# Kernel tuning notes

Measured on AMD Instinct MI355X. Metric: run time of the kernel, lower is better.

## Reference

```python
import jax, jax.numpy as jnp
import numpy as np
from jax import lax


def _conv1x1(x, w, b=None):
    # x: [N,C,H,W], w: [O,C]
    y = jnp.einsum('nchw,oc->nohw', x, w)
    if b is not None:
        y = y + b[None, :, None, None]
    return y


def _bn(x, g, b, rm, rv):
    # eval-mode BatchNorm2d, eps=1e-5 (torch default)
    inv = g / jnp.sqrt(rv + 1e-5)
    return x * inv[None, :, None, None] + (b - rm * inv)[None, :, None, None]


def setup_inputs() -> dict:
    key = jax.random.key(0)
    ks = jax.random.split(key, 32)
    N, C1, C2, H, W = 16, 256, 256, 64, 64
    mid = C2 // 16  # local_att reduction=16
    f32 = jnp.float32
    def nrm(k, shp, s=0.05):
        return s * jax.random.normal(k, shp, f32)
    return dict(
        x1=jax.random.normal(ks[0], (N, C1, H, W), f32),
        x2=jax.random.normal(ks[1], (N, C2, H, W), f32),
        conv1_w=nrm(ks[2], (C2, C1)), conv1_b=nrm(ks[3], (C2,)),
        conv2_w=nrm(ks[4], (C2, C2)), conv2_b=nrm(ks[5], (C2,)),
        conv3_w=nrm(ks[6], (C2, C2)), conv3_b=nrm(ks[7], (C2,)),
        conv4_w=nrm(ks[8], (C2, C2)), conv4_b=nrm(ks[9], (C2,)),
        conv4g_w=nrm(ks[10], (1, C2)), conv4g_b=nrm(ks[11], (1,)),
        bn_g=1.0 + nrm(ks[12], (C2,)), bn_b=nrm(ks[13], (C2,)),
        bn_rm=nrm(ks[14], (C2,)), bn_rv=1.0 + 0.1 * jax.random.uniform(ks[15], (C2,), f32),
        gamma=jax.random.normal(ks[16], (C2, 1, 1), f32), beta=jnp.zeros((C2, 1, 1), f32),
        gate_w=nrm(ks[17], (C2, C2)), gate_b=nrm(ks[18], (C2,)),
        dw_w=nrm(ks[19], (C2, 1, 3, 3)), dw_b=nrm(ks[20], (C2,)),
        interact_w=nrm(ks[21], (C2 // 4, C2 // 4)), interact_b=0.5 + nrm(ks[22], (C2 // 4,)),
        ca_w=nrm(ks[23], (1, 1, 5)),  # channel_att conv1d kernel, k=5 for C=256
        la1_w=nrm(ks[24], (mid, C2)),
        la_bn_g=1.0 + nrm(ks[25], (mid,)), la_bn_b=nrm(ks[26], (mid,)),
        la_bn_rm=nrm(ks[27], (mid,)), la_bn_rv=1.0 + 0.1 * jax.random.uniform(ks[28], (mid,), f32),
        fh_w=nrm(ks[29], (C2, mid)), fw_w=nrm(ks[30], (C2, mid)),
    )


def reference(x1, x2, conv1_w, conv1_b, conv2_w, conv2_b, conv3_w, conv3_b,
              conv4_w, conv4_b, conv4g_w, conv4g_b, bn_g, bn_b, bn_rm, bn_rv,
              gamma, beta, gate_w, gate_b, dw_w, dw_b, interact_w, interact_b,
              ca_w, la1_w, la_bn_g, la_bn_b, la_bn_rm, la_bn_rv, fh_w, fw_w):
    N, _, H, W = x1.shape
    C = conv1_w.shape[0]
    g1 = _conv1x1(x1, conv1_w, conv1_b)
    w1 = jax.nn.sigmoid(_bn(g1, bn_g, bn_b, bn_rm, bn_rv))
    g2 = _conv1x1(x2, conv2_w, conv2_b)
    w2 = jax.nn.sigmoid(_bn(g2, bn_g, bn_b, bn_rm, bn_rv))
    XG = g1 + g2

    # channel_att: GAP -> conv1d(k=5) across channels -> sigmoid gate
    y = XG.mean((2, 3))[:, None, :]  # [N,1,C]
    y = lax.conv_general_dilated(y, ca_w, (1,), [(2, 2)],
                                 dimension_numbers=('NCH', 'OIH', 'NCH'))
    temp = XG * jax.nn.sigmoid(y[:, 0, :])[:, :, None, None]

    # spatial sigmoid gate then 4-way group interact + softmax reweight
    Xs = jax.nn.sigmoid(_conv1x1(XG, conv4g_w, conv4g_b)) * XG
    C4 = C // 4
    Xr = Xs.reshape(N, 4, C4, H, W)
    o1 = jnp.einsum('ngchw,oc->ngohw', Xr, interact_w) + interact_b[None, None, :, None, None]
    xmap = o1.reshape(N, 4, 1, C4 * H * W)
    xav = xmap / xmap.mean(-1, keepdims=True)
    soft = jax.nn.softmax(xav, axis=2)  # softmax over size-1 dim -> ones (faithful)
    out = (soft.reshape(N, 4, C4, H, W) * Xr).reshape(N, C, H, W)

    # per-group (16) normalization using X_GOBAL stats (std unbiased, ddof=1)
    GN = 16
    xs = XG.reshape(N, GN, -1)
    mu = xs.mean(-1, keepdims=True)
    sd = jnp.std(xs, axis=-1, keepdims=True, ddof=1)
    x_gui = ((out.reshape(N, GN, -1) - mu) / (sd + 1e-10)).reshape(N, C, H, W)
    x_gui = x_gui * gamma[None] + beta[None]

    # threshold masks vs global-avg sigmoid reweights
    rw = jax.nn.sigmoid(XG.mean((2, 3), keepdims=True))  # [N,C,1,1]
    up1 = rw >= w1
    up2 = rw >= w2
    zero = jnp.zeros((), XG.dtype)
    x_up = jnp.where(up1, XG, zero) + jnp.where(up2, XG, zero)
    x_low = jnp.where(~up1, XG, zero) + jnp.where(~up2, XG, zero)

    # low branch: dwconv3x3 -> 1x1 -> channel-softmax gate
    dw = lax.conv_general_dilated(x_low, dw_w, (1, 1), [(1, 1), (1, 1)],
                                  dimension_numbers=('NCHW', 'OIHW', 'NCHW'),
                                  feature_group_count=C) + dw_b[None, :, None, None]
    x11 = _conv1x1(dw, conv3_w, conv3_b)
    gate = jax.nn.softmax(jax.nn.relu(x_low.mean((2, 3)) @ gate_w.T + gate_b), axis=1)
    xL = x11 * gate[:, :, None, None] + _conv1x1(x_up, conv4_w, conv4_b) + x_gui + temp

    # local_att (coordinate attention)
    xh = jnp.swapaxes(xL.mean(3, keepdims=True), 2, 3)  # [N,C,1,H]
    xw = xL.mean(2, keepdims=True)                       # [N,C,1,W]
    yc = jax.nn.relu(_bn(_conv1x1(jnp.concatenate([xh, xw], 3), la1_w),
                         la_bn_g, la_bn_b, la_bn_rm, la_bn_rv))
    sh = jax.nn.sigmoid(_conv1x1(jnp.swapaxes(yc[..., :H], 2, 3), fh_w))  # [N,C,H,1]
    sw = jax.nn.sigmoid(_conv1x1(yc[..., H:], fw_w))                      # [N,C,1,W]
    return xL * sh * sw
```

## Files before the change

### kernel.cpp

```cpp
#include <hip/hip_runtime.h>
#include <cstddef>
#include <cstdint>

constexpr int NN = 16, CC = 256, HH = 64, WW = 64, HW = 64 * 64;
constexpr size_t FSZ = (size_t)NN * CC * HW;

typedef short bf16x8 __attribute__((ext_vector_type(8)));
typedef float f32x4 __attribute__((ext_vector_type(4)));

__device__ __forceinline__ float sigmoidf_(float x) { return 1.f / (1.f + expf(-x)); }

__device__ __forceinline__ unsigned short bf16_rne(float f) {
    uint32_t u = __builtin_bit_cast(uint32_t, f);
    u += 0x7FFFu + ((u >> 16) & 1u);
    return (unsigned short)(u >> 16);
}
__device__ __forceinline__ float bf16_tof(unsigned short h) {
    uint32_t u = ((uint32_t)h) << 16;
    return __builtin_bit_cast(float, u);
}


__global__ __launch_bounds__(256) void wsplit_kernel(
    const float* __restrict__ w1, const float* __restrict__ w2,
    const float* __restrict__ w3, const float* __restrict__ w4,
    unsigned short* __restrict__ w1h, unsigned short* __restrict__ w1m, unsigned short* __restrict__ w1l,
    unsigned short* __restrict__ w2h, unsigned short* __restrict__ w2m, unsigned short* __restrict__ w2l,
    unsigned short* __restrict__ w4h, unsigned short* __restrict__ w4l,
    unsigned short* __restrict__ w3b,
    float* __restrict__ zstat, float* __restrict__ zspix) {
    const int i = blockIdx.x * 256 + threadIdx.x;
    const int o = i >> 8, c = i & 255;
    const size_t fo = ((size_t)((o >> 4) * 8 + (c >> 5))) * 512 +
                      (size_t)(((c & 31) >> 3) * 128 + (o & 15) * 8 + (c & 7));
    {
        float x = w1[i];
        unsigned short h = bf16_rne(x); float r = x - bf16_tof(h);
        unsigned short m = bf16_rne(r); float r2 = r - bf16_tof(m);
        w1h[fo] = h; w1m[fo] = m; w1l[fo] = bf16_rne(r2);
    }
    {
        float x = w2[i];
        unsigned short h = bf16_rne(x); float r = x - bf16_tof(h);
        unsigned short m = bf16_rne(r); float r2 = r - bf16_tof(m);
        w2h[fo] = h; w2m[fo] = m; w2l[fo] = bf16_rne(r2);
    }
    {
        float x = w4[i];
        unsigned short h = bf16_rne(x); float r = x - bf16_tof(h);
        w4h[fo] = h; w4l[fo] = bf16_rne(r);
    }
    w3b[fo] = bf16_rne(w3[i]);
    if (i < 8192) zstat[i] = 0.f;
    zspix[i] = 0.f;
}

template <int NS>
__global__ __launch_bounds__(256) void tsplit_kernel(const float* __restrict__ X,
                                                     unsigned short* __restrict__ O0,
                                                     unsigned short* __restrict__ O1,
                                                     unsigned short* __restrict__ O2) {
    const int hw0 = blockIdx.x * 64, c0 = blockIdx.y * 64, n = blockIdx.z;
    __shared__ float sT[64][65];
    const int tid = threadIdx.x;
    {
        const int hwl = (tid & 15) << 2;
        const int cl = tid >> 4;
#pragma unroll
        for (int p = 0; p < 4; ++p) {
            const int c = cl + p * 16;
            const float4 v = *(const float4*)(X + ((size_t)(n * CC + c0 + c)) * HW + hw0 + hwl);
            sT[c][hwl] = v.x; sT[c][hwl + 1] = v.y; sT[c][hwl + 2] = v.z; sT[c][hwl + 3] = v.w;
        }
    }
    __syncthreads();
    const int hwl = tid >> 2, cb = (tid & 3) << 4;
    unsigned short h[16], m[16], l[16];
#pragma unroll
    for (int j = 0; j < 16; ++j) {
        const float x = sT[cb + j][hwl];
        const unsigned short hh = bf16_rne(x);
        h[j] = hh;
        if (NS >= 2) {
            const float r = x - bf16_tof(hh);
            const unsigned short mm = bf16_rne(r);
            m[j] = mm;
            if (NS >= 3) l[j] = bf16_rne(r - bf16_tof(mm));
        }
    }
    const size_t ob = ((size_t)(n * HW + hw0 + hwl)) * 256 + c0 + cb;
    *(int4*)(O0 + ob) = *(int4*)&h[0]; *(int4*)(O0 + ob + 8) = *(int4*)&h[8];
    if (NS >= 2) { *(int4*)(O1 + ob) = *(int4*)&m[0]; *(int4*)(O1 + ob + 8) = *(int4*)&m[8]; }
    if (NS >= 3) { *(int4*)(O2 + ob) = *(int4*)&l[0]; *(int4*)(O2 + ob + 8) = *(int4*)&l[8]; }
}

template <int NS>
__device__ __forceinline__ void mfma_core4(const unsigned short* __restrict__ X0,
                                           const unsigned short* __restrict__ X1,
                                           const unsigned short* __restrict__ X2,
                                           const unsigned short* __restrict__ W0,
                                           const unsigned short* __restrict__ W1,
                                           const unsigned short* __restrict__ W2,
                                           int n, int hw0, int o0, f32x4 (&acc)[2][4]) {
    __shared__ unsigned short sX[2][NS][64][40];
    const int tid = threadIdx.x;
    const int lane = tid & 63, wv = tid >> 6, quad = lane >> 4, nlo = lane & 15;
    const int srow = tid >> 2, skoff = (tid & 3) << 3;
    const unsigned short* Xs[3] = {X0, X1, X2};
    const unsigned short* Ws[3] = {W0, W1, W2};
    const size_t xg = ((size_t)(n * HW + hw0 + srow)) * 256 + skoff;
    const unsigned short* wp[NS];
#pragma unroll
    for (int s = 0; s < NS; ++s)
        wp[s] = Ws[s] + ((size_t)((o0 >> 4) + wv) * 8) * 512 + (size_t)lane * 8;

#pragma unroll
    for (int s = 0; s < NS; ++s)
        *(int4*)&sX[0][s][srow][skoff] = *(const int4*)(Xs[s] + xg);
    __syncthreads();

    for (int ks = 0; ks < 8; ++ks) {
        const int cur = ks & 1;
        int4 nx[NS];
        if (ks < 7) {
#pragma unroll
            for (int s = 0; s < NS; ++s) nx[s] = *(const int4*)(Xs[s] + xg + (ks + 1) * 32);
        }
        bf16x8 af[NS][2];
#pragma unroll
        for (int s = 0; s < NS; ++s)
#pragma unroll
            for (int f = 0; f < 2; ++f)
                af[s][f] = *(const bf16x8*)(wp[s] + ((size_t)(f * 32 + ks)) * 512);
#pragma unroll
        for (int nt = 0; nt < 4; ++nt) {
            bf16x8 bfr[NS];
#pragma unroll
            for (int s = 0; s < NS; ++s) bfr[s] = *(const bf16x8*)&sX[cur][s][nt * 16 + nlo][quad * 8];
#pragma unroll
            for (int f = 0; f < 2; ++f) {
                if (NS == 3) {
                    acc[f][nt] = __builtin_amdgcn_mfma_f32_16x16x32_bf16(af[1][f], bfr[1], acc[f][nt], 0, 0, 0);
                    acc[f][nt] = __builtin_amdgcn_mfma_f32_16x16x32_bf16(af[0][f], bfr[2], acc[f][nt], 0, 0, 0);
                    acc[f][nt] = __builtin_amdgcn_mfma_f32_16x16x32_bf16(af[2][f], bfr[0], acc[f][nt], 0, 0, 0);
                    acc[f][nt] = __builtin_amdgcn_mfma_f32_16x16x32_bf16(af[0][f], bfr[1], acc[f][nt], 0, 0, 0);
                    acc[f][nt] = __builtin_amdgcn_mfma_f32_16x16x32_bf16(af[1][f], bfr[0], acc[f][nt], 0, 0, 0);
                    acc[f][nt] = __builtin_amdgcn_mfma_f32_16x16x32_bf16(af[0][f], bfr[0], acc[f][nt], 0, 0, 0);
                } else if (NS == 2) {
                    acc[f][nt] = __builtin_amdgcn_mfma_f32_16x16x32_bf16(af[0][f], bfr[1], acc[f][nt], 0, 0, 0);
                    acc[f][nt] = __builtin_amdgcn_mfma_f32_16x16x32_bf16(af[1][f], bfr[0], acc[f][nt], 0, 0, 0);
                    acc[f][nt] = __builtin_amdgcn_mfma_f32_16x16x32_bf16(af[0][f], bfr[0], acc[f][nt], 0, 0, 0);
                } else {
                    acc[f][nt] = __builtin_amdgcn_mfma_f32_16x16x32_bf16(af[0][f], bfr[0], acc[f][nt], 0, 0, 0);
                }
            }
        }
        if (ks < 7) {
#pragma unroll
            for (int s = 0; s < NS; ++s) *(int4*)&sX[cur ^ 1][s][srow][skoff] = nx[s];
        }
        __syncthreads();
    }
}

template <int NS>
__global__ __launch_bounds__(256, 3) void gemm_mfma_kernel(
    const unsigned short* __restrict__ X0, const unsigned short* __restrict__ X1,
    const unsigned short* __restrict__ X2, const unsigned short* __restrict__ W0,
    const unsigned short* __restrict__ W1, const unsigned short* __restrict__ W2,
    const float* __restrict__ bias, float* __restrict__ Y) {
    const int hw0 = blockIdx.x * 64, o0 = blockIdx.y * 128, n = blockIdx.z;
    f32x4 acc[2][4] = {};
    mfma_core4<NS>(X0, X1, X2, W0, W1, W2, n, hw0, o0, acc);
    const int lane = threadIdx.x & 63, wv = threadIdx.x >> 6;
    const int quad = lane >> 4, nlo = lane & 15;
#pragma unroll
    for (int f = 0; f < 2; ++f) {
        const int om = o0 + f * 64 + wv * 16 + quad * 4;
#pragma unroll
        for (int nt = 0; nt < 4; ++nt) {
            const int hw = hw0 + nt * 16 + nlo;
#pragma unroll
            for (int r = 0; r < 4; ++r) {
                const int o = om + r;
                Y[((size_t)(n * CC + o)) * HW + hw] = acc[f][nt][r] + bias[o];
            }
        }
    }
}

__global__ __launch_bounds__(256, 3) void gemm_xg_kernel(
    const unsigned short* __restrict__ X0, const unsigned short* __restrict__ X1,
    const unsigned short* __restrict__ X2, const unsigned short* __restrict__ W0,
    const unsigned short* __restrict__ W1, const unsigned short* __restrict__ W2,
    const float* __restrict__ bias, const float* __restrict__ g1,
    const float* __restrict__ cgw,
    float* __restrict__ XG, float* __restrict__ sum_c, float* __restrict__ sq_c,
    float* __restrict__ s_pix) {
    const int hw0 = blockIdx.x * 64, o0 = blockIdx.y * 128, n = blockIdx.z;
    f32x4 acc[2][4] = {};
    mfma_core4<3>(X0, X1, X2, W0, W1, W2, n, hw0, o0, acc);
    __shared__ float sRed[4][64];
    const int lane = threadIdx.x & 63, wv = threadIdx.x >> 6;
    const int quad = lane >> 4, nlo = lane & 15;
    float pnt[4] = {0.f, 0.f, 0.f, 0.f};
#pragma unroll
    for (int f = 0; f < 2; ++f) {
        const int om = o0 + f * 64 + wv * 16 + quad * 4;
#pragma unroll
        for (int r = 0; r < 4; ++r) {
            const int o = om + r;
            const float b = bias[o];
            const float wg = cgw[o];
            float s = 0.f, q = 0.f;
#pragma unroll
            for (int nt = 0; nt < 4; ++nt) {
                const int hw = hw0 + nt * 16 + nlo;
                const size_t rowi = ((size_t)(n * CC + o)) * HW + hw;
                const float xg = acc[f][nt][r] + b + g1[rowi];
                XG[rowi] = xg;
                s += xg; q += xg * xg;
                pnt[nt] += wg * xg;
            }
#pragma unroll
            for (int off = 1; off < 16; off <<= 1) { s += __shfl_xor(s, off); q += __shfl_xor(q, off); }
            if (nlo == 0) { atomicAdd(&sum_c[n * CC + o], s); atomicAdd(&sq_c[n * CC + o], q); }
        }
    }
#pragma unroll
    for (int nt = 0; nt < 4; ++nt) {
        float p = pnt[nt];
        p += __shfl_xor(p, 16); p += __shfl_xor(p, 32);
        if (quad == 0) sRed[wv][nt * 16 + nlo] = p;
    }
    __syncthreads();
    if (threadIdx.x < 64) {
        const float s2 = sRed[0][threadIdx.x] + sRed[1][threadIdx.x] +
                         sRed[2][threadIdx.x] + sRed[3][threadIdx.x];
        atomicAdd(&s_pix[n * HW + hw0 + threadIdx.x], s2);
    }
}

__global__ __launch_bounds__(256, 3) void gemm_final_kernel(
    const unsigned short* __restrict__ X0, const unsigned short* __restrict__ W0,
    const float* __restrict__ bias,
    const float* __restrict__ A, const float* __restrict__ XG, const float* __restrict__ s_pix,
    const float* __restrict__ cgb,
    const float* __restrict__ gate, const float* __restrict__ ca_sig,
    const float* __restrict__ mu_g, const float* __restrict__ isd_g,
    const float* __restrict__ gamma, const float* __restrict__ beta,
    float* __restrict__ out) {
    const int hw0 = blockIdx.x * 64, o0 = blockIdx.y * 128, n = blockIdx.z;
    f32x4 acc[2][4] = {};
    mfma_core4<1>(X0, nullptr, nullptr, W0, nullptr, nullptr, n, hw0, o0, acc);
    const int lane = threadIdx.x & 63, wv = threadIdx.x >> 6;
    const int quad = lane >> 4, nlo = lane & 15;
    const float cgb0 = cgb[0];
#pragma unroll
    for (int f = 0; f < 2; ++f) {
        const int om = o0 + f * 64 + wv * 16 + quad * 4;
#pragma unroll
        for (int nt = 0; nt < 4; ++nt) {
            const int hw = hw0 + nt * 16 + nlo;
            const int pix = n * HW + hw;
            const float sp = sigmoidf_(s_pix[pix] + cgb0);
#pragma unroll
            for (int r = 0; r < 4; ++r) {
                const int o = om + r;
                const float g = gate[n * CC + o];
                const float cs = ca_sig[n * CC + o];
                const float mu = mu_g[n * 16 + (o >> 4)];
                const float isd = isd_g[n * 16 + (o >> 4)];
                const size_t rowi = ((size_t)(n * CC + o)) * HW + hw;
                const float xg = XG[rowi];
                const float gui = (sp * xg - mu) * isd * gamma[o] + beta[o];
                out[rowi] = (acc[f][nt][r] + bias[o]) * g + A[rowi] + gui + xg * cs;
            }
        }
    }
}

__global__ __launch_bounds__(256) void stats2_kernel(const float* __restrict__ sum_c,
                                                     const float* __restrict__ sq_c,
                                                     const float* __restrict__ caw,
                                                     float* __restrict__ rw,
                                                     float* __restrict__ ca_sig,
                                                     float* __restrict__ mu_g,
                                                     float* __restrict__ isd_g,
                                                     float* __restrict__ xlow_sum) {
    const int n = blockIdx.x, c = threadIdx.x;
    __shared__ float m[256];
    const float mean = sum_c[n * CC + c] * (1.f / (float)HW);
    m[c] = mean;
    rw[n * CC + c] = sigmoidf_(mean);
    xlow_sum[n * CC + c] = 0.f;
    __syncthreads();
    float y = 0.f;
#pragma unroll
    for (int k = 0; k < 5; ++k) {
        const int cc = c - 2 + k;
        if (cc >= 0 && cc < 256) y += m[cc] * caw[k];
    }
    ca_sig[n * CC + c] = sigmoidf_(y);
    if (c < 16) {
        float S = 0.f, Q = 0.f;
        for (int j = 0; j < 16; ++j) {
            S += sum_c[n * CC + c * 16 + j];
            Q += sq_c[n * CC + c * 16 + j];
        }
        const float cnt = 65536.f;
        const float mu = S / cnt;
        float var = (Q - S * S / cnt) * (1.f / (cnt - 1.f));
        var = fmaxf(var, 0.f);
        mu_g[n * 16 + c] = mu;
        isd_g[n * 16 + c] = 1.f / (sqrtf(var) + 1e-10f);
    }
}

__global__ __launch_bounds__(256) void masks_split_kernel(
    float* g1_xlow,
    const float* __restrict__ XG,
    const float* __restrict__ rw,
    const float* __restrict__ bng, const float* __restrict__ bnb,
    const float* __restrict__ bnrm, const float* __restrict__ bnrv,
    unsigned short* __restrict__ O0, unsigned short* __restrict__ O1,
    float* __restrict__ xlow_sum) {
    const int hw0 = blockIdx.x * 64, c0 = blockIdx.y * 64, n = blockIdx.z;
    __shared__ float sT[64][65];
    const int tid = threadIdx.x;
    const int cl = tid >> 2;
    const int q = tid & 3;
    const int c = c0 + cl;
    const float inv = bng[c] / sqrtf(bnrv[c] + 1e-5f);
    const float off = bnb[c] - bnrm[c] * inv;
    const float rwv = rw[n * CC + c];
    const size_t rowb = ((size_t)(n * CC + c)) * HW + hw0;
    float lsum = 0.f;
#pragma unroll
    for (int j = 0; j < 4; ++j) {
        const int hwl = q * 4 + j * 16;
        const float4 a = *(const float4*)(g1_xlow + rowb + hwl);
        const float4 x = *(const float4*)(XG + rowb + hwl);
        const float* ap = &a.x; const float* xp = &x.x;
        float4 xlv;
        float* xlp = &xlv.x;
#pragma unroll
        for (int e = 0; e < 4; ++e) {
            const float g2e = xp[e] - ap[e];
            const float w1 = sigmoidf_(inv * ap[e] + off);
            const float w2 = sigmoidf_(inv * g2e + off);
            const float cu = (rwv >= w1 ? 1.f : 0.f) + (rwv >= w2 ? 1.f : 0.f);
            const float xu = xp[e] * cu;
            const float xl = xp[e] * (2.f - cu);
            sT[cl][hwl + e] = xu;
            xlp[e] = xl;
            lsum += xl;
        }
        *(float4*)(g1_xlow + rowb + hwl) = xlv;
    }
    lsum += __shfl_xor(lsum, 1);
    lsum += __shfl_xor(lsum, 2);
    if (q == 0) atomicAdd(&xlow_sum[n * CC + c], lsum);
    __syncthreads();
    const int hwl2 = tid >> 2, cb = (tid & 3) << 4;
    unsigned short h[16], m[16];
#pragma unroll
    for (int j = 0; j < 16; ++j) {
        const float x = sT[cb + j][hwl2];
        const unsigned short hh = bf16_rne(x);
        h[j] = hh;
        m[j] = bf16_rne(x - bf16_tof(hh));
    }
    const size_t ob = ((size_t)(n * HW + hw0 + hwl2)) * 256 + c0 + cb;
    *(int4*)(O0 + ob) = *(int4*)&h[0]; *(int4*)(O0 + ob + 8) = *(int4*)&h[8];
    *(int4*)(O1 + ob) = *(int4*)&m[0]; *(int4*)(O1 + ob + 8) = *(int4*)&m[8];
}

__global__ __launch_bounds__(256) void gate_kernel(const float* __restrict__ xlow_sum,
                                                   const float* __restrict__ gatew,
                                                   const float* __restrict__ gateb,
                                                   float* __restrict__ gate) {
    const int n = blockIdx.x, c = threadIdx.x;
    __shared__ float xm[256];
    __shared__ float red[256];
    xm[c] = xlow_sum[n * CC + c] * (1.f / (float)HW);
    __syncthreads();
    float acc = gateb[c];
    const float* wr = gatew + (size_t)c * 256;
#pragma unroll 8
    for (int k = 0; k < 256; ++k) acc += xm[k] * wr[k];
    const float v = fmaxf(acc, 0.f);
    red[c] = v;
    __syncthreads();
    for (int s = 128; s > 0; s >>= 1) {
        if (c < s) red[c] = fmaxf(red[c], red[c + s]);
        __syncthreads();
    }
    const float mx = red[0];
    __syncthreads();
    const float e = expf(v - mx);
    red[c] = e;
    __syncthreads();
    for (int s = 128; s > 0; s >>= 1) {
        if (c < s) red[c] += red[c + s];
        __syncthreads();
    }
    gate[n * CC + c] = e / red[0];
}

__global__ __launch_bounds__(256) void dwconv_kernel(const float* __restrict__ xlow,
                                                     const float* __restrict__ dww,
                                                     const float* __restrict__ dwb,
                                                     float* __restrict__ out) {
    const int c = blockIdx.x & 255;
    __shared__ float sl[64][65];
    const size_t base = (size_t)blockIdx.x * HW;
    for (int r = 0; r < 16; ++r) {
        const int idx = threadIdx.x + r * 256;
        sl[idx >> 6][idx & 63] = xlow[base + idx];
    }
    float wk[9];
#pragma unroll
    for (int j = 0; j < 9; ++j) wk[j] = dww[c * 9 + j];
    const float bias = dwb[c];
    __syncthreads();
    for (int r = 0; r < 16; ++r) {
        const int idx = threadIdx.x + r * 256;
        const int h = idx >> 6, w = idx & 63;
        float acc = bias;
#pragma unroll
        for (int dh = 0; dh < 3; ++dh) {
            const int hh = h + dh - 1;
            if (hh < 0 || hh > 63) continue;
#pragma unroll
            for (int dw2 = 0; dw2 < 3; ++dw2) {
                const int ww2 = w + dw2 - 1;
                if (ww2 < 0 || ww2 > 63) continue;
                acc += sl[hh][ww2] * wk[dh * 3 + dw2];
            }
        }
        out[base + idx] = acc;
    }
}

__global__ __launch_bounds__(256) void pool_kernel(const float* __restrict__ xL,
                                                   float* __restrict__ xh,
                                                   float* __restrict__ xw) {
    __shared__ float sl[64][65];
    const size_t base = (size_t)blockIdx.x * HW;
    for (int r = 0; r < 16; ++r) {
        const int idx = threadIdx.x + r * 256;
        sl[idx >> 6][idx & 63] = xL[base + idx];
    }
    __syncthreads();
    const int t = threadIdx.x;
    if (t < 64) {
        float s = 0.f;
        for (int w = 0; w < 64; ++w) s += sl[t][w];
        xh[(size_t)blockIdx.x * 64 + t] = s * (1.f / 64.f);
    } else if (t < 128) {
        const int w = t - 64;
        float s = 0.f;
        for (int h = 0; h < 64; ++h) s += sl[h][w];
        xw[(size_t)blockIdx.x * 64 + w] = s * (1.f / 64.f);
    }
}

__global__ __launch_bounds__(256) void local_att_kernel(const float* __restrict__ xh,
                                                        const float* __restrict__ xw,
                                                        const float* __restrict__ la1w,
                                                        const float* __restrict__ lag,
                                                        const float* __restrict__ lab,
                                                        const float* __restrict__ larm,
                                                        const float* __restrict__ larv,
                                                        const float* __restrict__ fhw,
                                                        const float* __restrict__ fww,
                                                        float* __restrict__ sh,
                                                        float* __restrict__ sw) {
    const int n = blockIdx.x;
    __shared__ float w1s[16 * 256];
    __shared__ float fhs[256 * 16];
    __shared__ float fws[256 * 16];
    __shared__ float ycs[16][128];
    for (int i = threadIdx.x; i < 4096; i += 256) {
        w1s[i] = la1w[i];
        fhs[i] = fhw[i];
        fws[i] = fww[i];
    }
    __syncthreads();
    for (int idx = threadIdx.x; idx < 2048; idx += 256) {
        const int m = idx >> 7, p = idx & 127;
        const float* vsrc = (p < 64) ? (xh + (size_t)n * CC * 64 + p)
                                     : (xw + (size_t)n * CC * 64 + (p - 64));
        float acc = 0.f;
#pragma unroll 8
        for (int c = 0; c < 256; ++c) acc += w1s[m * 256 + c] * vsrc[(size_t)c * 64];
        const float inv = lag[m] / sqrtf(larv[m] + 1e-5f);
        const float off = lab[m] - larm[m] * inv;
        ycs[m][p] = fmaxf(inv * acc + off, 0.f);
    }
    __syncthreads();
    for (int idx = threadIdx.x; idx < 16384; idx += 256) {
        const int c = idx >> 6, h = idx & 63;
        float a1 = 0.f, a2 = 0.f;
#pragma unroll
        for (int m = 0; m < 16; ++m) {
            a1 += fhs[c * 16 + m] * ycs[m][h];
            a2 += fws[c * 16 + m] * ycs[m][64 + h];
        }
        sh[(size_t)n * CC * 64 + idx] = sigmoidf_(a1);
        sw[(size_t)n * CC * 64 + idx] = sigmoidf_(a2);
    }
}

__global__ __launch_bounds__(256) void final_kernel(float* __restrict__ out,
                                                    const float* __restrict__ sh,
                                                    const float* __restrict__ sw) {
    __shared__ float shs[64], sws[64];
    const int t = threadIdx.x;
    if (t < 64) shs[t] = sh[(size_t)blockIdx.x * 64 + t];
    else if (t < 128) sws[t - 64] = sw[(size_t)blockIdx.x * 64 + (t - 64)];
    __syncthreads();
    const size_t base = (size_t)blockIdx.x * HW;
#pragma unroll 4
    for (int r = 0; r < 16; ++r) {
        const int idx = t + r * 256;
        out[base + idx] *= shs[idx >> 6] * sws[idx & 63];
    }
}

extern "C" void kernel_launch(void* const* d_in, const int* in_sizes, int n_in,
                              void* d_out, int out_size, void* d_ws, size_t ws_size,
                              hipStream_t stream) {
    const float* x1 = (const float*)d_in[0];
    const float* x2 = (const float*)d_in[1];
    const float* c1w = (const float*)d_in[2];
    const float* c1b = (const float*)d_in[3];
    const float* c2w = (const float*)d_in[4];
    const float* c2b = (const float*)d_in[5];
    const float* c3w = (const float*)d_in[6];
    const float* c3b = (const float*)d_in[7];
    const float* c4w = (const float*)d_in[8];
    const float* c4b = (const float*)d_in[9];
    const float* cgw = (const float*)d_in[10];
    const float* cgb = (const float*)d_in[11];
    const float* bng = (const float*)d_in[12];
    const float* bnb = (const float*)d_in[13];
    const float* bnrm = (const float*)d_in[14];
    const float* bnrv = (const float*)d_in[15];
    const float* gamma = (const float*)d_in[16];
    const float* beta = (const float*)d_in[17];
    const float* gatew = (const float*)d_in[18];
    const float* gateb = (const float*)d_in[19];
    const float* dww = (const float*)d_in[20];
    const float* dwb = (const float*)d_in[21];
    const float* caw = (const float*)d_in[24];
    const float* la1w = (const float*)d_in[25];
    const float* lag = (const float*)d_in[26];
    const float* lab = (const float*)d_in[27];
    const float* larm = (const float*)d_in[28];
    const float* larv = (const float*)d_in[29];
    const float* fhw = (const float*)d_in[30];
    const float* fww = (const float*)d_in[31];

    float* ws = (float*)d_ws;
    float* buf0 = ws;
    float* buf1 = ws + FSZ;
    float* buf2 = ws + 2 * FSZ;
    float* sp = ws + 3 * FSZ;
    float* sum_c = sp;    sp += 4096;
    float* sq_c = sp;     sp += 4096;
    float* rw = sp;       sp += 4096;
    float* ca_sig = sp;   sp += 4096;
    float* xlow_sum = sp; sp += 4096;
    float* mu_g = sp;     sp += 256;
    float* isd_g = sp;    sp += 256;
    float* s_pix = sp;    sp += (size_t)NN * HW;
    float* xh = sp;       sp += (size_t)NN * CC * 64;
    float* xwb = sp;      sp += (size_t)NN * CC * 64;
    float* shb = sp;      sp += (size_t)NN * CC * 64;
    float* swb = sp;      sp += (size_t)NN * CC * 64;
    unsigned short* wsp = (unsigned short*)shb;
    unsigned short* w1h = wsp + 0 * 65536;
    unsigned short* w1m = wsp + 1 * 65536;
    unsigned short* w1l = wsp + 2 * 65536;
    unsigned short* w2h = wsp + 3 * 65536;
    unsigned short* w2m = wsp + 4 * 65536;
    unsigned short* w2l = wsp + 5 * 65536;
    unsigned short* w4h = wsp + 6 * 65536;
    unsigned short* w4l = wsp + 7 * 65536;
    unsigned short* w3b = wsp + 8 * 65536;

    float* out = (float*)d_out;

    const dim3 gt(HW / 64, CC / 64, NN);
    const dim3 gg(HW / 64, CC / 128, NN);

    wsplit_kernel<<<256, 256, 0, stream>>>(c1w, c2w, c3w, c4w, w1h, w1m, w1l,
                                           w2h, w2m, w2l, w4h, w4l, w3b,
                                           sum_c, s_pix);
    {
        unsigned short* sx0 = (unsigned short*)buf1;
        unsigned short* sx1 = (unsigned short*)buf1 + FSZ;
        unsigned short* sx2 = (unsigned short*)buf2;
        tsplit_kernel<3><<<gt, 256, 0, stream>>>(x1, sx0, sx1, sx2);
        gemm_mfma_kernel<3><<<gg, 256, 0, stream>>>(sx0, sx1, sx2, w1h, w1m, w1l, c1b, buf0);
    }
    {
        unsigned short* sx0 = (unsigned short*)out;
        unsigned short* sx1 = (unsigned short*)out + FSZ;
        unsigned short* sx2 = (unsigned short*)buf2;
        tsplit_kernel<3><<<gt, 256, 0, stream>>>(x2, sx0, sx1, sx2);
        gemm_xg_kernel<<<gg, 256, 0, stream>>>(sx0, sx1, sx2, w2h, w2m, w2l, c2b,
                                               buf0, cgw, buf1, sum_c, sq_c, s_pix);
    }
    stats2_kernel<<<NN, 256, 0, stream>>>(sum_c, sq_c, caw, rw, ca_sig, mu_g, isd_g, xlow_sum);
    {
        unsigned short* ux0 = (unsigned short*)out;
        unsigned short* ux1 = (unsigned short*)out + FSZ;
        masks_split_kernel<<<gt, 256, 0, stream>>>(buf0, buf1, rw, bng, bnb, bnrm, bnrv,
                                                   ux0, ux1, xlow_sum);
    }
    float* gate = sum_c;
    gate_kernel<<<NN, 256, 0, stream>>>(xlow_sum, gatew, gateb, gate);
    dwconv_kernel<<<NN * CC, 256, 0, stream>>>(buf0, dww, dwb, buf2);
    {
        unsigned short* sx0 = (unsigned short*)buf0;
        tsplit_kernel<1><<<gt, 256, 0, stream>>>(buf2, sx0, nullptr, nullptr);
    }
    {
        unsigned short* ux0 = (unsigned short*)out;
        unsigned short* ux1 = (unsigned short*)out + FSZ;
        gemm_mfma_kernel<2><<<gg, 256, 0, stream>>>(ux0, ux1, nullptr, w4h, w4l, nullptr,
                                                    c4b, buf2);
    }
    {
        unsigned short* sx0 = (unsigned short*)buf0;
        gemm_final_kernel<<<gg, 256, 0, stream>>>(sx0, w3b, c3b, buf2, buf1, s_pix, cgb,
                                                  gate, ca_sig, mu_g, isd_g, gamma, beta, out);
    }
    pool_kernel<<<NN * CC, 256, 0, stream>>>(out, xh, xwb);
    local_att_kernel<<<NN, 256, 0, stream>>>(xh, xwb, la1w, lag, lab, larm, larv,
                                             fhw, fww, shb, swb);
    final_kernel<<<NN * CC, 256, 0, stream>>>(out, shb, swb);
}
```

Baseline: 653.0 us.

## Fuse conv4 and conv3 GEMMs into one final kernel sharing the tile loop

Merges the separate conv4 GEMM (split-bf16 x_up) into the final GEMM kernel so that both the conv3 and conv4 products are accumulated in one pass with a shared double-buffered LDS pipeline. This removes writing the fp32 conv4 result to global memory and reading it back, and drops one kernel launch. Buffers are reshuffled: dwconv now writes in place into buf0, the xL result goes to buf0, and final_kernel writes to out. The cost is more accumulator registers (two 2x4 f32x4 sets) and three LDS slices, which may lower occupancy under the launch bound of 3.

Measured after the change: 669.4 us. 1.03x slower.

```diff
diff --git a/kernel.cpp b/kernel.cpp
--- a/kernel.cpp
+++ b/kernel.cpp
@@ -163,6 +163,65 @@
     }
 }
 
+__device__ __forceinline__ void mfma_core_pair(const unsigned short* __restrict__ XUH,
+                                               const unsigned short* __restrict__ XUL,
+                                               const unsigned short* __restrict__ XDW,
+                                               const unsigned short* __restrict__ W4H,
+                                               const unsigned short* __restrict__ W4L,
+                                               const unsigned short* __restrict__ W3B,
+                                               int n, int hw0, int o0,
+                                               f32x4 (&acc_a)[2][4], f32x4 (&acc_b)[2][4]) {
+    __shared__ unsigned short sX[2][3][64][40];
+    const int tid = threadIdx.x;
+    const int lane = tid & 63, wv = tid >> 6, quad = lane >> 4, nlo = lane & 15;
+    const int srow = tid >> 2, skoff = (tid & 3) << 3;
+    const unsigned short* Xs[3] = {XUH, XUL, XDW};
+    const unsigned short* Ws[3] = {W4H, W4L, W3B};
+    const size_t xg = ((size_t)(n * HW + hw0 + srow)) * 256 + skoff;
+    const unsigned short* wp[3];
+#pragma unroll
+    for (int s = 0; s < 3; ++s)
+        wp[s] = Ws[s] + ((size_t)((o0 >> 4) + wv) * 8) * 512 + (size_t)lane * 8;
+
+#pragma unroll
+    for (int s = 0; s < 3; ++s)
+        *(int4*)&sX[0][s][srow][skoff] = *(const int4*)(Xs[s] + xg);
+    __syncthreads();
+
+    for (int ks = 0; ks < 8; ++ks) {
+        const int cur = ks & 1;
+        int4 nx[3];
+        if (ks < 7) {
+#pragma unroll
+            for (int s = 0; s < 3; ++s) nx[s] = *(const int4*)(Xs[s] + xg + (ks + 1) * 32);
+        }
+        bf16x8 af[3][2];
+#pragma unroll
+        for (int s = 0; s < 3; ++s)
+#pragma unroll
+            for (int f = 0; f < 2; ++f)
+                af[s][f] = *(const bf16x8*)(wp[s] + ((size_t)(f * 32 + ks)) * 512);
+#pragma unroll
+        for (int nt = 0; nt < 4; ++nt) {
+            bf16x8 bfr[3];
+#pragma unroll
+            for (int s = 0; s < 3; ++s) bfr[s] = *(const bf16x8*)&sX[cur][s][nt * 16 + nlo][quad * 8];
+#pragma unroll
+            for (int f = 0; f < 2; ++f) {
+                acc_a[f][nt] = __builtin_amdgcn_mfma_f32_16x16x32_bf16(af[0][f], bfr[1], acc_a[f][nt], 0, 0, 0);
+                acc_a[f][nt] = __builtin_amdgcn_mfma_f32_16x16x32_bf16(af[1][f], bfr[0], acc_a[f][nt], 0, 0, 0);
+                acc_a[f][nt] = __builtin_amdgcn_mfma_f32_16x16x32_bf16(af[0][f], bfr[0], acc_a[f][nt], 0, 0, 0);
+                acc_b[f][nt] = __builtin_amdgcn_mfma_f32_16x16x32_bf16(af[2][f], bfr[2], acc_b[f][nt], 0, 0, 0);
+            }
+        }
+        if (ks < 7) {
+#pragma unroll
+            for (int s = 0; s < 3; ++s) *(int4*)&sX[cur ^ 1][s][srow][skoff] = nx[s];
+        }
+        __syncthreads();
+    }
+}
+
 template <int NS>
 __global__ __launch_bounds__(256, 3) void gemm_mfma_kernel(
     const unsigned short* __restrict__ X0, const unsigned short* __restrict__ X1,
@@ -217,10 +276,10 @@
             for (int nt = 0; nt < 4; ++nt) {
                 const int hw = hw0 + nt * 16 + nlo;
                 const size_t rowi = ((size_t)(n * CC + o)) * HW + hw;
-                const float xg = acc[f][nt][r] + b + g1[rowi];
-                XG[rowi] = xg;
-                s += xg; q += xg * xg;
-                pnt[nt] += wg * xg;
+                const float xgv = acc[f][nt][r] + b + g1[rowi];
+                XG[rowi] = xgv;
+                s += xgv; q += xgv * xgv;
+                pnt[nt] += wg * xgv;
             }
 #pragma unroll
             for (int off = 1; off < 16; off <<= 1) { s += __shfl_xor(s, off); q += __shfl_xor(q, off); }
@@ -242,17 +301,21 @@
 }
 
 __global__ __launch_bounds__(256, 3) void gemm_final_kernel(
-    const unsigned short* __restrict__ X0, const unsigned short* __restrict__ W0,
-    const float* __restrict__ bias,
-    const float* __restrict__ A, const float* __restrict__ XG, const float* __restrict__ s_pix,
+    const unsigned short* __restrict__ XUH, const unsigned short* __restrict__ XUL,
+    const unsigned short* __restrict__ XDW,
+    const unsigned short* __restrict__ W4H, const unsigned short* __restrict__ W4L,
+    const unsigned short* __restrict__ W3B,
+    const float* __restrict__ b3, const float* __restrict__ b4,
+    const float* __restrict__ XG, const float* __restrict__ s_pix,
     const float* __restrict__ cgb,
     const float* __restrict__ gate, const float* __restrict__ ca_sig,
     const float* __restrict__ mu_g, const float* __restrict__ isd_g,
     const float* __restrict__ gamma, const float* __restrict__ beta,
     float* __restrict__ out) {
     const int hw0 = blockIdx.x * 64, o0 = blockIdx.y * 128, n = blockIdx.z;
-    f32x4 acc[2][4] = {};
-    mfma_core4<1>(X0, nullptr, nullptr, W0, nullptr, nullptr, n, hw0, o0, acc);
+    f32x4 acc_a[2][4] = {};
+    f32x4 acc_b[2][4] = {};
+    mfma_core_pair(XUH, XUL, XDW, W4H, W4L, W3B, n, hw0, o0, acc_a, acc_b);
     const int lane = threadIdx.x & 63, wv = threadIdx.x >> 6;
     const int quad = lane >> 4, nlo = lane & 15;
     const float cgb0 = cgb[0];
@@ -274,7 +337,7 @@
                 const size_t rowi = ((size_t)(n * CC + o)) * HW + hw;
                 const float xg = XG[rowi];
                 const float gui = (sp * xg - mu) * isd * gamma[o] + beta[o];
-                out[rowi] = (acc[f][nt][r] + bias[o]) * g + A[rowi] + gui + xg * cs;
+                out[rowi] = (acc_b[f][nt][r] + b3[o]) * g + (acc_a[f][nt][r] + b4[o]) + gui + xg * cs;
             }
         }
     }
@@ -513,9 +576,10 @@
     }
 }
 
-__global__ __launch_bounds__(256) void final_kernel(float* __restrict__ out,
+__global__ __launch_bounds__(256) void final_kernel(const float* __restrict__ xL,
                                                     const float* __restrict__ sh,
-                                                    const float* __restrict__ sw) {
+                                                    const float* __restrict__ sw,
+                                                    float* __restrict__ out) {
     __shared__ float shs[64], sws[64];
     const int t = threadIdx.x;
     if (t < 64) shs[t] = sh[(size_t)blockIdx.x * 64 + t];
@@ -525,7 +589,7 @@
 #pragma unroll 4
     for (int r = 0; r < 16; ++r) {
         const int idx = t + r * 256;
-        out[base + idx] *= shs[idx >> 6] * sws[idx & 63];
+        out[base + idx] = xL[base + idx] * shs[idx >> 6] * sws[idx & 63];
     }
 }
 
@@ -623,24 +687,22 @@
     }
     float* gate = sum_c;
     gate_kernel<<<NN, 256, 0, stream>>>(xlow_sum, gatew, gateb, gate);
-    dwconv_kernel<<<NN * CC, 256, 0, stream>>>(buf0, dww, dwb, buf2);
-    {
-        unsigned short* sx0 = (unsigned short*)buf0;
-        tsplit_kernel<1><<<gt, 256, 0, stream>>>(buf2, sx0, nullptr, nullptr);
+    dwconv_kernel<<<NN * CC, 256, 0, stream>>>(buf0, dww, dwb, buf0);
+    {
+        unsigned short* sx0 = (unsigned short*)buf2;
+        tsplit_kernel<1><<<gt, 256, 0, stream>>>(buf0, sx0, nullptr, nullptr);
     }
     {
         unsigned short* ux0 = (unsigned short*)out;
         unsigned short* ux1 = (unsigned short*)out + FSZ;
-        gemm_mfma_kernel<2><<<gg, 256, 0, stream>>>(ux0, ux1, nullptr, w4h, w4l, nullptr,
-                                                    c4b, buf2);
-    }
-    {
-        unsigned short* sx0 = (unsigned short*)buf0;
-        gemm_final_kernel<<<gg, 256, 0, stream>>>(sx0, w3b, c3b, buf2, buf1, s_pix, cgb,
-                                                  gate, ca_sig, mu_g, isd_g, gamma, beta, out);
-    }
-    pool_kernel<<<NN * CC, 256, 0, stream>>>(out, xh, xwb);
+        unsigned short* sx0 = (unsigned short*)buf2;
+        gemm_final_kernel<<<gg, 256, 0, stream>>>(ux0, ux1, sx0, w4h, w4l, w3b,
+                                                  c3b, c4b, buf1, s_pix, cgb,
+                                                  gate, ca_sig, mu_g, isd_g, gamma, beta,
+                                                  buf0);
+    }
+    pool_kernel<<<NN * CC, 256, 0, stream>>>(buf0, xh, xwb);
     local_att_kernel<<<NN, 256, 0, stream>>>(xh, xwb, la1w, lag, lab, larm, larv,
                                              fhw, fww, shb, swb);
-    final_kernel<<<NN * CC, 256, 0, stream>>>(out, shb, swb);
-}
+    final_kernel<<<NN * CC, 256, 0, stream>>>(buf0, shb, swb, out);
+}
```
